# Kernel tuning notes

Hardware: AMD Instinct MI355X
Metric: run time of the kernel (lower is better)

The kernel has to match this reference:

```python
import jax, jax.numpy as jnp
import numpy as np

B, T, D, HS = 4, 4096, 1024, 64


def setup_inputs() -> dict:
    key = jax.random.key(0)
    k1, k2, k3 = jax.random.split(key, 3)
    x = jax.random.normal(k1, (B, T, D), dtype=jnp.float32)
    # Linear(n_embd, head_size, bias=False) weights: [head_size, n_embd]
    Wk = jax.random.normal(k2, (HS, D), dtype=jnp.float32) * (D ** -0.5)
    Wv = jax.random.normal(k3, (HS, D), dtype=jnp.float32) * (D ** -0.5)
    return {"x": x, "Wk": Wk, "Wv": Wv}


def reference(x, Wk, Wv):
    # Faithful to source: q = self.value(x) (query proj is dead code), so q and v
    # share the value projection.
    k = jnp.einsum('btd,hd->bth', x, Wk)   # [B,T,HS]
    qv = jnp.einsum('btd,hd->bth', x, Wv)  # [B,T,HS]; serves as both q and v
    scale = k.shape[-1] ** -0.5
    scores = jnp.einsum('bth,bsh->bts', qv, k) * scale  # [B,T,T]
    causal = jnp.tril(jnp.ones((T, T), dtype=bool))
    scores = jnp.where(causal, scores, -jnp.inf)
    weights = jax.nn.softmax(scores, axis=-1)
    out = jnp.einsum('bts,bsh->bth', weights, qv)  # [B,T,HS]
    return out
```

## Files before the change

### kernel.cpp

```cpp
#include <hip/hip_runtime.h>
#include <hip/hip_bf16.h>

typedef __bf16 bf16;
typedef __attribute__((ext_vector_type(8))) __bf16 bf16x8;
typedef __attribute__((ext_vector_type(4))) float f32x4;

#define T_SEQ 4096
#define D_EMB 1024
#define HS 64

__device__ __forceinline__ float fexp2(float x) {
#if __has_builtin(__builtin_amdgcn_exp2f)
    return __builtin_amdgcn_exp2f(x);
#else
    return exp2f(x);
#endif
}

__global__ __launch_bounds__(256) void wcast_kernel(
    const float* __restrict__ Wk, const float* __restrict__ Wv,
    bf16* __restrict__ wbf)
{
    const int t = blockIdx.x * 256 + threadIdx.x;
    const int base = t * 8;
    const float* src = (base < 65536) ? (Wk + base) : (Wv + base - 65536);
    float4 f0 = *(const float4*)(src);
    float4 f1 = *(const float4*)(src + 4);
    bf16x8 o = {(__bf16)f0.x, (__bf16)f0.y, (__bf16)f0.z, (__bf16)f0.w,
                (__bf16)f1.x, (__bf16)f1.y, (__bf16)f1.z, (__bf16)f1.w};
    *(bf16x8*)(wbf + base) = o;
}

__global__ __launch_bounds__(256) void proj_kernel(
    const float* __restrict__ x,
    const bf16* __restrict__ wbf,
    bf16* __restrict__ kmat,
    bf16* __restrict__ qvmat,
    bf16* __restrict__ qvT)
{
    __shared__ float red[4][2048];

    const int lane = threadIdx.x & 63;
    const int wave = threadIdx.x >> 6;
    const int col  = lane & 15;
    const int quad = lane >> 4;
    const int rowbase = blockIdx.x * 16;

    const float* xrow = x + (size_t)(rowbase + col) * D_EMB + wave * 256;

    f32x4 acc[8];
#pragma unroll
    for (int i = 0; i < 8; ++i) acc[i] = {0.f, 0.f, 0.f, 0.f};

    for (int k0 = 0; k0 < 256; k0 += 32) {
        float4 a0 = *(const float4*)(xrow + k0 + quad * 8);
        float4 a1 = *(const float4*)(xrow + k0 + quad * 8 + 4);
        bf16x8 a = {(__bf16)a0.x, (__bf16)a0.y, (__bf16)a0.z, (__bf16)a0.w,
                    (__bf16)a1.x, (__bf16)a1.y, (__bf16)a1.z, (__bf16)a1.w};
#pragma unroll
        for (int nt = 0; nt < 8; ++nt) {
            const bf16* wrow = wbf + (size_t)(nt * 16 + col) * D_EMB + wave * 256;
            bf16x8 b = *(const bf16x8*)(wrow + k0 + quad * 8);
            acc[nt] = __builtin_amdgcn_mfma_f32_16x16x32_bf16(a, b, acc[nt], 0, 0, 0);
        }
    }

#pragma unroll
    for (int nt = 0; nt < 8; ++nt)
        *(f32x4*)&red[wave][nt * 256 + lane * 4] = acc[nt];
    __syncthreads();

    const int t = threadIdx.x;
    f32x4 s0 = {0.f,0.f,0.f,0.f}, s1 = {0.f,0.f,0.f,0.f};
#pragma unroll
    for (int w = 0; w < 4; ++w) {
        s0 += *(const f32x4*)&red[w][t * 8];
        s1 += *(const f32x4*)&red[w][t * 8 + 4];
    }
    const int nt = t >> 5;
    const int L0 = (t & 31) * 2;
#pragma unroll
    for (int j2 = 0; j2 < 2; ++j2) {
        const int L  = L0 + j2;
        const int q  = L >> 4;
        const int cc = L & 15;
        const int c  = (nt & 3) * 16 + cc;
        f32x4 v = j2 ? s1 : s0;
#pragma unroll
        for (int r = 0; r < 4; ++r) {
            const int grow = rowbase + q * 4 + r;
            bf16 bv = (bf16)v[r];
            if (nt < 4) {
                kmat[(size_t)grow * HS + c] = bv;
            } else {
                qvmat[(size_t)grow * HS + c] = bv;
                const int bb = grow >> 12;
                const int tt = grow & (T_SEQ - 1);
                qvT[((size_t)bb * HS + c) * T_SEQ + tt] = bv;
            }
        }
    }
}

__global__ __launch_bounds__(256, 3) void attn_kernel(
    const bf16* __restrict__ kmat,
    const bf16* __restrict__ qvmat,
    const bf16* __restrict__ qvT,
    float* __restrict__ out,
    float* __restrict__ o_parts,
    float* __restrict__ l_parts)
{
    __shared__ bf16 Kt[2][64][72];
    __shared__ bf16 Vt[2][64][72];
    __shared__ bf16 plds[4][16][40];

    const int tid  = threadIdx.x;
    const int lane = tid & 63;
    const int wave = tid >> 6;
    const int col  = lane & 15;
    const int quad = lane >> 4;

    const int b = blockIdx.x / 288;
    const int r = blockIdx.x - b * 288;
    int a = 0;
    while (4 * (a + 1) * (a + 2) <= r) ++a;
    const int rr = r - 4 * a * (a + 1);
    const int m  = rr / (a + 1);
    const int jc = rr - m * (a + 1);
    const int qb = 8 * a + m;

    const int cbeg  = jc * 8;
    const int nctot = qb + 1;
    const int cend  = (nctot < cbeg + 8) ? nctot : cbeg + 8;

    const bf16* qvb = qvmat + (size_t)b * T_SEQ * HS;
    const bf16* kb  = kmat  + (size_t)b * T_SEQ * HS;
    const bf16* vTb = qvT   + (size_t)b * HS * T_SEQ;

    const int q0 = qb * 64 + wave * 16;

    bf16x8 qf0 = *(const bf16x8*)(qvb + (size_t)(q0 + col) * HS + quad * 8);
    bf16x8 qf1 = *(const bf16x8*)(qvb + (size_t)(q0 + col) * HS + 32 + quad * 8);

    f32x4 o[4];
    float lp[4];
#pragma unroll
    for (int h = 0; h < 4; ++h) o[h] = {0.f, 0.f, 0.f, 0.f};
#pragma unroll
    for (int rr2 = 0; rr2 < 4; ++rr2) lp[rr2] = 0.f;

    const float sc = 0.125f * 1.44269504088896f;

    {
        const int kc = cbeg * 64;
#pragma unroll
        for (int it = 0; it < 2; ++it) {
            const int idx = it * 256 + tid;
            const int kr  = idx >> 3;
            const int off = (idx & 7) * 8;
            bf16x8 kv = *(const bf16x8*)(kb + (size_t)kc * HS + idx * 8);
            bf16x8 vv = *(const bf16x8*)(vTb + (size_t)kr * T_SEQ + kc + off);
            *(bf16x8*)&Kt[0][kr][off] = kv;
            *(bf16x8*)&Vt[0][kr][off] = vv;
        }
    }
    __syncthreads();

    int buf = 0;
#pragma unroll 1
    for (int c = cbeg; c < cend; ++c) {
        const bool more = (c + 1 < cend);

        bf16x8 kn[2], vn[2];
        if (more) {
            const int kcn = (c + 1) * 64;
#pragma unroll
            for (int it = 0; it < 2; ++it) {
                const int idx = it * 256 + tid;
                const int kr  = idx >> 3;
                const int off = (idx & 7) * 8;
                kn[it] = *(const bf16x8*)(kb + (size_t)kcn * HS + idx * 8);
                vn[it] = *(const bf16x8*)(vTb + (size_t)kr * T_SEQ + kcn + off);
            }
        }

        const int kc = c * 64;
#pragma unroll
        for (int st = 0; st < 2; ++st) {
            const int gk = kc + 32 * st;
            if (gk > q0 + 15) break;

            bf16x8 b0 = *(const bf16x8*)&Kt[buf][32 * st + col][quad * 8];
            bf16x8 b1 = *(const bf16x8*)&Kt[buf][32 * st + col][32 + quad * 8];
            bf16x8 b2 = *(const bf16x8*)&Kt[buf][32 * st + 16 + col][quad * 8];
            bf16x8 b3 = *(const bf16x8*)&Kt[buf][32 * st + 16 + col][32 + quad * 8];

            float p[2][4];
            {
                f32x4 a4 = {0.f, 0.f, 0.f, 0.f};
                a4 = __builtin_amdgcn_mfma_f32_16x16x32_bf16(qf0, b0, a4, 0, 0, 0);
                a4 = __builtin_amdgcn_mfma_f32_16x16x32_bf16(qf1, b1, a4, 0, 0, 0);
#pragma unroll
                for (int i = 0; i < 4; ++i) p[0][i] = fexp2(fmaf(a4[i], sc, -24.f));
            }
            {
                f32x4 a4 = {0.f, 0.f, 0.f, 0.f};
                a4 = __builtin_amdgcn_mfma_f32_16x16x32_bf16(qf0, b2, a4, 0, 0, 0);
                a4 = __builtin_amdgcn_mfma_f32_16x16x32_bf16(qf1, b3, a4, 0, 0, 0);
#pragma unroll
                for (int i = 0; i < 4; ++i) p[1][i] = fexp2(fmaf(a4[i], sc, -24.f));
            }

            if (gk + 31 > q0) {
#pragma unroll
                for (int nt = 0; nt < 2; ++nt)
#pragma unroll
                    for (int i = 0; i < 4; ++i)
                        if (gk + nt * 16 + col > q0 + quad * 4 + i)
                            p[nt][i] = 0.f;
            }

#pragma unroll
            for (int i = 0; i < 4; ++i) lp[i] += p[0][i] + p[1][i];

#pragma unroll
            for (int nt = 0; nt < 2; ++nt)
#pragma unroll
                for (int i = 0; i < 4; ++i)
                    plds[wave][quad * 4 + i][nt * 16 + col] = (bf16)p[nt][i];
            bf16x8 pa = *(const bf16x8*)&plds[wave][col][quad * 8];

#pragma unroll
            for (int h = 0; h < 4; ++h) {
                bf16x8 vb = *(const bf16x8*)&Vt[buf][h * 16 + col][32 * st + quad * 8];
                o[h] = __builtin_amdgcn_mfma_f32_16x16x32_bf16(pa, vb, o[h], 0, 0, 0);
            }
        }

        if (more) {
#pragma unroll
            for (int it = 0; it < 2; ++it) {
                const int idx = it * 256 + tid;
                const int kr  = idx >> 3;
                const int off = (idx & 7) * 8;
                *(bf16x8*)&Kt[buf ^ 1][kr][off] = kn[it];
                *(bf16x8*)&Vt[buf ^ 1][kr][off] = vn[it];
            }
            __syncthreads();
            buf ^= 1;
        }
    }

    float lr[4];
#pragma unroll
    for (int i = 0; i < 4; ++i) {
        float v = lp[i];
#pragma unroll
        for (int off = 1; off < 16; off <<= 1)
            v += __shfl_xor(v, off, 64);
        lr[i] = v;
    }

    const size_t rowbase = (size_t)b * T_SEQ + q0 + quad * 4;
    if (col == 0) {
#pragma unroll
        for (int i = 0; i < 4; ++i)
            l_parts[(size_t)jc * 16384 + rowbase + i] = lr[i];
    }

    float* dst = (jc == 0) ? out : (o_parts + (size_t)(jc - 1) * 16384 * HS);
#pragma unroll
    for (int h = 0; h < 4; ++h)
#pragma unroll
        for (int i = 0; i < 4; ++i)
            dst[(rowbase + i) * HS + h * 16 + col] = o[h][i];
}

__global__ __launch_bounds__(256) void norm_kernel(
    float* __restrict__ out,
    const float* __restrict__ o_parts,
    const float* __restrict__ l_parts)
{
    const int i   = blockIdx.x * 256 + threadIdx.x;
    const int row = i >> 6;
    const int qb  = (row & 4095) >> 6;
    const int nj  = (qb >> 3) + 1;

    float s = out[i];
    float L = l_parts[row];
    for (int j = 1; j < nj; ++j) {
        s += o_parts[(size_t)(j - 1) * 1048576 + i];
        L += l_parts[(size_t)j * 16384 + row];
    }
    out[i] = s / L;
}

extern "C" void kernel_launch(void* const* d_in, const int* in_sizes, int n_in,
                              void* d_out, int out_size, void* d_ws, size_t ws_size,
                              hipStream_t stream) {
    const float* x  = (const float*)d_in[0];
    const float* Wk = (const float*)d_in[1];
    const float* Wv = (const float*)d_in[2];
    float* out = (float*)d_out;

    bf16* ws    = (bf16*)d_ws;
    bf16* wbf   = ws;
    bf16* kmat  = ws + (size_t)128 * 1024;
    bf16* qvmat = kmat + (size_t)16384 * 64;
    bf16* qvT   = qvmat + (size_t)16384 * 64;
    float* o_parts = (float*)(qvT + (size_t)16384 * 64);
    float* l_parts = o_parts + (size_t)7 * 16384 * 64;

    wcast_kernel<<<64, 256, 0, stream>>>(Wk, Wv, wbf);
    proj_kernel<<<1024, 256, 0, stream>>>(x, wbf, kmat, qvmat, qvT);
    attn_kernel<<<1152, 256, 0, stream>>>(kmat, qvmat, qvT, out, o_parts, l_parts);
    norm_kernel<<<4096, 256, 0, stream>>>(out, o_parts, l_parts);
}
```

Measured before the change: 165.1 us.

## Retile projection GEMM with LDS-staged double-buffered x and weight tiles

The projection kernel now computes 64 rows per block with all 128 output columns. x and weight tiles are staged through double-buffered shared memory, with register prefetch of the next K chunk, replacing the earlier split-K design that needed a per-block LDS reduction. Each weight tile is reused across four times more rows, which cuts redundant weight traffic and removes the reduction step. The risk is that only 256 blocks launch, which may underfill the GPU and lower the memory-level parallelism for streaming x.

```diff
diff --git a/kernel.cpp b/kernel.cpp
--- a/kernel.cpp
+++ b/kernel.cpp
@@ -2,6 +2,7 @@
 #include <hip/hip_bf16.h>
 
 typedef __bf16 bf16;
+typedef __attribute__((ext_vector_type(4))) __bf16 bf16x4;
 typedef __attribute__((ext_vector_type(8))) __bf16 bf16x8;
 typedef __attribute__((ext_vector_type(4))) float f32x4;
 
@@ -31,75 +32,134 @@
     *(bf16x8*)(wbf + base) = o;
 }
 
-__global__ __launch_bounds__(256) void proj_kernel(
+__global__ __launch_bounds__(256, 2) void proj_kernel(
     const float* __restrict__ x,
     const bf16* __restrict__ wbf,
     bf16* __restrict__ kmat,
     bf16* __restrict__ qvmat,
     bf16* __restrict__ qvT)
 {
-    __shared__ float red[4][2048];
-
-    const int lane = threadIdx.x & 63;
-    const int wave = threadIdx.x >> 6;
+    __shared__ bf16 xs[2][64][72];
+    __shared__ bf16 ws[2][128][72];
+
+    const int tid  = threadIdx.x;
+    const int lane = tid & 63;
+    const int wave = tid >> 6;
     const int col  = lane & 15;
     const int quad = lane >> 4;
-    const int rowbase = blockIdx.x * 16;
-
-    const float* xrow = x + (size_t)(rowbase + col) * D_EMB + wave * 256;
-
-    f32x4 acc[8];
-#pragma unroll
-    for (int i = 0; i < 8; ++i) acc[i] = {0.f, 0.f, 0.f, 0.f};
-
-    for (int k0 = 0; k0 < 256; k0 += 32) {
-        float4 a0 = *(const float4*)(xrow + k0 + quad * 8);
-        float4 a1 = *(const float4*)(xrow + k0 + quad * 8 + 4);
-        bf16x8 a = {(__bf16)a0.x, (__bf16)a0.y, (__bf16)a0.z, (__bf16)a0.w,
-                    (__bf16)a1.x, (__bf16)a1.y, (__bf16)a1.z, (__bf16)a1.w};
-#pragma unroll
-        for (int nt = 0; nt < 8; ++nt) {
-            const bf16* wrow = wbf + (size_t)(nt * 16 + col) * D_EMB + wave * 256;
-            bf16x8 b = *(const bf16x8*)(wrow + k0 + quad * 8);
-            acc[nt] = __builtin_amdgcn_mfma_f32_16x16x32_bf16(a, b, acc[nt], 0, 0, 0);
-        }
-    }
-
-#pragma unroll
-    for (int nt = 0; nt < 8; ++nt)
-        *(f32x4*)&red[wave][nt * 256 + lane * 4] = acc[nt];
+    const int rowbase = blockIdx.x * 64;
+
+    f32x4 acc[4][2];
+#pragma unroll
+    for (int mt = 0; mt < 4; ++mt)
+#pragma unroll
+        for (int nt = 0; nt < 2; ++nt) acc[mt][nt] = {0.f, 0.f, 0.f, 0.f};
+
+    {
+#pragma unroll
+        for (int p = 0; p < 4; ++p) {
+            const int idx = p * 256 + tid;
+            const int xr  = idx >> 4;
+            const int c4  = (idx & 15) * 4;
+            float4 f = *(const float4*)(x + (size_t)(rowbase + xr) * D_EMB + c4);
+            bf16x4 v = {(__bf16)f.x, (__bf16)f.y, (__bf16)f.z, (__bf16)f.w};
+            *(bf16x4*)&xs[0][xr][c4] = v;
+        }
+#pragma unroll
+        for (int p = 0; p < 4; ++p) {
+            const int idx = p * 256 + tid;
+            const int wr  = idx >> 3;
+            const int off = (idx & 7) * 8;
+            *(bf16x8*)&ws[0][wr][off] = *(const bf16x8*)(wbf + (size_t)wr * D_EMB + off);
+        }
+    }
     __syncthreads();
 
-    const int t = threadIdx.x;
-    f32x4 s0 = {0.f,0.f,0.f,0.f}, s1 = {0.f,0.f,0.f,0.f};
-#pragma unroll
-    for (int w = 0; w < 4; ++w) {
-        s0 += *(const f32x4*)&red[w][t * 8];
-        s1 += *(const f32x4*)&red[w][t * 8 + 4];
-    }
-    const int nt = t >> 5;
-    const int L0 = (t & 31) * 2;
-#pragma unroll
-    for (int j2 = 0; j2 < 2; ++j2) {
-        const int L  = L0 + j2;
-        const int q  = L >> 4;
-        const int cc = L & 15;
-        const int c  = (nt & 3) * 16 + cc;
-        f32x4 v = j2 ? s1 : s0;
-#pragma unroll
-        for (int r = 0; r < 4; ++r) {
-            const int grow = rowbase + q * 4 + r;
-            bf16 bv = (bf16)v[r];
-            if (nt < 4) {
-                kmat[(size_t)grow * HS + c] = bv;
-            } else {
-                qvmat[(size_t)grow * HS + c] = bv;
-                const int bb = grow >> 12;
-                const int tt = grow & (T_SEQ - 1);
-                qvT[((size_t)bb * HS + c) * T_SEQ + tt] = bv;
-            }
-        }
-    }
+    int buf = 0;
+#pragma unroll 1
+    for (int c = 0; c < 16; ++c) {
+        const bool more = (c + 1 < 16);
+
+        float4 xn[4];
+        bf16x8 wn[4];
+        if (more) {
+            const int k0 = (c + 1) * 64;
+#pragma unroll
+            for (int p = 0; p < 4; ++p) {
+                const int idx = p * 256 + tid;
+                const int xr  = idx >> 4;
+                const int c4  = (idx & 15) * 4;
+                xn[p] = *(const float4*)(x + (size_t)(rowbase + xr) * D_EMB + k0 + c4);
+            }
+#pragma unroll
+            for (int p = 0; p < 4; ++p) {
+                const int idx = p * 256 + tid;
+                const int wr  = idx >> 3;
+                const int off = (idx & 7) * 8;
+                wn[p] = *(const bf16x8*)(wbf + (size_t)wr * D_EMB + k0 + off);
+            }
+        }
+
+#pragma unroll
+        for (int s = 0; s < 2; ++s) {
+            bf16x8 af[4];
+#pragma unroll
+            for (int mt = 0; mt < 4; ++mt)
+                af[mt] = *(const bf16x8*)&xs[buf][mt * 16 + col][s * 32 + quad * 8];
+            bf16x8 bfr[2];
+#pragma unroll
+            for (int nt = 0; nt < 2; ++nt)
+                bfr[nt] = *(const bf16x8*)&ws[buf][wave * 32 + nt * 16 + col][s * 32 + quad * 8];
+#pragma unroll
+            for (int mt = 0; mt < 4; ++mt)
+#pragma unroll
+                for (int nt = 0; nt < 2; ++nt)
+                    acc[mt][nt] = __builtin_amdgcn_mfma_f32_16x16x32_bf16(
+                        af[mt], bfr[nt], acc[mt][nt], 0, 0, 0);
+        }
+
+        if (more) {
+#pragma unroll
+            for (int p = 0; p < 4; ++p) {
+                const int idx = p * 256 + tid;
+                const int xr  = idx >> 4;
+                const int c4  = (idx & 15) * 4;
+                bf16x4 v = {(__bf16)xn[p].x, (__bf16)xn[p].y,
+                            (__bf16)xn[p].z, (__bf16)xn[p].w};
+                *(bf16x4*)&xs[buf ^ 1][xr][c4] = v;
+            }
+#pragma unroll
+            for (int p = 0; p < 4; ++p) {
+                const int idx = p * 256 + tid;
+                const int wr  = idx >> 3;
+                const int off = (idx & 7) * 8;
+                *(bf16x8*)&ws[buf ^ 1][wr][off] = wn[p];
+            }
+            __syncthreads();
+            buf ^= 1;
+        }
+    }
+
+#pragma unroll
+    for (int mt = 0; mt < 4; ++mt)
+#pragma unroll
+        for (int nt = 0; nt < 2; ++nt) {
+            const int gcol = wave * 32 + nt * 16 + col;
+#pragma unroll
+            for (int r = 0; r < 4; ++r) {
+                const int grow = rowbase + mt * 16 + quad * 4 + r;
+                bf16 bv = (bf16)acc[mt][nt][r];
+                if (gcol < 64) {
+                    kmat[(size_t)grow * HS + gcol] = bv;
+                } else {
+                    const int h = gcol - 64;
+                    qvmat[(size_t)grow * HS + h] = bv;
+                    const int bb = grow >> 12;
+                    const int tt = grow & (T_SEQ - 1);
+                    qvT[((size_t)bb * HS + h) * T_SEQ + tt] = bv;
+                }
+            }
+        }
 }
 
 __global__ __launch_bounds__(256, 3) void attn_kernel(
@@ -147,7 +207,7 @@
 #pragma unroll
     for (int h = 0; h < 4; ++h) o[h] = {0.f, 0.f, 0.f, 0.f};
 #pragma unroll
-    for (int rr2 = 0; rr2 < 4; ++rr2) lp[rr2] = 0.f;
+    for (int i = 0; i < 4; ++i) lp[i] = 0.f;
 
     const float sc = 0.125f * 1.44269504088896f;
 
@@ -312,7 +372,7 @@
     float* l_parts = o_parts + (size_t)7 * 16384 * 64;
 
     wcast_kernel<<<64, 256, 0, stream>>>(Wk, Wv, wbf);
-    proj_kernel<<<1024, 256, 0, stream>>>(x, wbf, kmat, qvmat, qvT);
+    proj_kernel<<<256, 256, 0, stream>>>(x, wbf, kmat, qvmat, qvT);
     attn_kernel<<<1152, 256, 0, stream>>>(kmat, qvmat, qvT, out, o_parts, l_parts);
     norm_kernel<<<4096, 256, 0, stream>>>(out, o_parts, l_parts);
 }
```

Measured after the change: 151.2 us. 1.09x faster.
